# Kernel tuning notes

Hardware: AMD Instinct MI355X
Metric: run time of the kernel (lower is better)

## Reference

```python
import jax, jax.numpy as jnp
import numpy as np
import math

B, S, H, DM, DFF = 8, 512, 16, 1024, 4096
DK = DM // H
EPS = 1e-6


def setup_inputs() -> dict:
    key = jax.random.key(0)
    ks = jax.random.split(key, 12)
    rn = lambda k, shape, s=0.02: (jax.random.normal(k, shape, jnp.float32) * s)
    return dict(
        x=jax.random.normal(ks[0], (B, S, DM), jnp.float32),
        mask=jnp.ones((B, 1, 1, S), jnp.int32),
        Wq=rn(ks[1], (DM, DM)), bq=jnp.zeros((DM,), jnp.float32),
        Wk=rn(ks[2], (DM, DM)), bk=jnp.zeros((DM,), jnp.float32),
        Wv=rn(ks[3], (DM, DM)), bv=jnp.zeros((DM,), jnp.float32),
        Wo=rn(ks[4], (DM, DM)), bo=jnp.zeros((DM,), jnp.float32),
        r_k=rn(ks[5], (S, S, DK)),
        r_v=rn(ks[6], (S, S, DK)),
        ln1_g=jnp.ones((DM,), jnp.float32), ln1_b=jnp.zeros((DM,), jnp.float32),
        ln2_g=jnp.ones((DM,), jnp.float32), ln2_b=jnp.zeros((DM,), jnp.float32),
        w1=rn(ks[7], (DFF, DM)), b1=jnp.zeros((DFF,), jnp.float32),
        w2=rn(ks[8], (DM, DFF)), b2=jnp.zeros((DM,), jnp.float32),
    )


def _layernorm(x, g, b):
    # torch: std with Bessel correction (ddof=1), divide by (std + eps)
    mean = jnp.mean(x, axis=-1, keepdims=True)
    std = jnp.std(x, axis=-1, keepdims=True, ddof=1)
    return g * (x - mean) / (std + EPS) + b


def _gelu_tanh(x):
    c = math.sqrt(2.0 / math.pi)
    return 0.5 * x * (1.0 + jnp.tanh(c * (x + 0.044715 * x * x * x)))


def _attention(xn, mask, Wq, bq, Wk, bk, Wv, bv, Wo, bo, r_k, r_v):
    def heads(x, W, bias):
        y = x @ W.T + bias                      # [B,S,DM]
        return y.reshape(B, S, H, DK).transpose(0, 2, 1, 3)  # [B,H,S,DK]
    q, k, v = heads(xn, Wq, bq), heads(xn, Wk, bk), heads(xn, Wv, bv)
    scale = 1.0 / math.sqrt(DK)
    scores = jnp.einsum('bhqd,bhkd->bhqk', q, k) * scale
    rel_score = jnp.einsum('bhqd,qkd->bhqk', q, r_k)  # relative-position bias
    scores = scores + rel_score * scale
    scores = jnp.where(mask == 0, -1e9, scores)
    p = jax.nn.softmax(scores, axis=-1)
    out = jnp.einsum('bhqk,bhkd->bhqd', p, v) + jnp.einsum('bhqk,qkd->bhqd', p, r_v)
    out = out.transpose(0, 2, 1, 3).reshape(B, S, DM)
    return out @ Wo.T + bo


def reference(x, mask, Wq, bq, Wk, bk, Wv, bv, Wo, bo, r_k, r_v,
              ln1_g, ln1_b, ln2_g, ln2_b, w1, b1, w2, b2):
    # sublayer 1: x + attn(LN(x))
    x = x + _attention(_layernorm(x, ln1_g, ln1_b), mask,
                       Wq, bq, Wk, bk, Wv, bv, Wo, bo, r_k, r_v)
    # sublayer 2: x + FFN(LN(x))
    h = _layernorm(x, ln2_g, ln2_b)
    h = _gelu_tanh(h @ w1.T + b1) @ w2.T + b2
    return x + h
```

## Files before the change

### kernel.cpp

```cpp
#include <hip/hip_runtime.h>
#include <math.h>


typedef unsigned short ushort_t;
typedef __attribute__((ext_vector_type(8))) short short8;
typedef __attribute__((ext_vector_type(4))) float f32x4;
typedef __attribute__((ext_vector_type(8))) __bf16 bf16x8;

__device__ __forceinline__ float b2f(ushort_t u) {
  unsigned v = (unsigned)u << 16;
  return __builtin_bit_cast(float, v);
}
__device__ __forceinline__ ushort_t f2b(float f) {
  unsigned x = __builtin_bit_cast(unsigned, f);
  x = x + 0x7fffu + ((x >> 16) & 1u);
  return (ushort_t)(x >> 16);
}

__device__ __forceinline__ void gload16(const ushort_t* g, ushort_t* l) {
  __builtin_amdgcn_global_load_lds(
      (const __attribute__((address_space(1))) unsigned*)g,
      (__attribute__((address_space(3))) unsigned*)l, 16, 0, 0);
}

__global__ void k_f32_to_bf16(const float* __restrict__ in,
                              ushort_t* __restrict__ out, long long n) {
  long long i = ((long long)blockIdx.x * blockDim.x + threadIdx.x) * 4;
  if (i >= n) return;
  float4 v = *reinterpret_cast<const float4*>(in + i);
  ushort4 o;
  o.x = f2b(v.x); o.y = f2b(v.y); o.z = f2b(v.z); o.w = f2b(v.w);
  *reinterpret_cast<ushort4*>(out + i) = o;
}

__global__ void k_layernorm_bf16(const float* __restrict__ x,
                                 const float* __restrict__ g,
                                 const float* __restrict__ b,
                                 ushort_t* __restrict__ out) {
  const int lane = threadIdx.x & 63;
  const int row = (blockIdx.x << 2) + (threadIdx.x >> 6);
  const float* xr = x + (long long)row * 1024;
  float4 v[4];
  float s = 0.f, ss = 0.f;
#pragma unroll
  for (int i = 0; i < 4; ++i) {
    v[i] = *reinterpret_cast<const float4*>(xr + lane * 16 + i * 4);
    s += v[i].x + v[i].y + v[i].z + v[i].w;
    ss += v[i].x * v[i].x + v[i].y * v[i].y + v[i].z * v[i].z + v[i].w * v[i].w;
  }
#pragma unroll
  for (int o = 32; o > 0; o >>= 1) {
    s += __shfl_xor(s, o);
    ss += __shfl_xor(ss, o);
  }
  float mean = s * (1.f / 1024.f);
  float var = (ss - 1024.f * mean * mean) * (1.f / 1023.f);
  var = fmaxf(var, 0.f);
  float inv = 1.f / (sqrtf(var) + 1e-6f);
  ushort_t* orow = out + (long long)row * 1024;
#pragma unroll
  for (int i = 0; i < 4; ++i) {
    int c = lane * 16 + i * 4;
    ushort4 o;
    o.x = f2b(g[c + 0] * (v[i].x - mean) * inv + b[c + 0]);
    o.y = f2b(g[c + 1] * (v[i].y - mean) * inv + b[c + 1]);
    o.z = f2b(g[c + 2] * (v[i].z - mean) * inv + b[c + 2]);
    o.w = f2b(g[c + 3] * (v[i].w - mean) * inv + b[c + 3]);
    *reinterpret_cast<ushort4*>(orow + c) = o;
  }
}

__global__ void k_softmax(ushort_t* __restrict__ sc, const int* __restrict__ mask,
                          float scale) {
  const int lane = threadIdx.x & 63;
  const long long row = ((long long)blockIdx.x << 2) + (threadIdx.x >> 6);
  const int b = (int)(row >> 13);
  ushort_t* srow = sc + row * 512;
  const int* mrow = mask + b * 512;
  short8 sv = *reinterpret_cast<const short8*>(srow + lane * 8);
  float vals[8];
  float mx = -1e30f;
#pragma unroll
  for (int j = 0; j < 8; ++j) {
    float f = b2f((ushort_t)sv[j]) * scale;
    if (mrow[lane * 8 + j] == 0) f = -1e9f;
    vals[j] = f;
    mx = fmaxf(mx, f);
  }
#pragma unroll
  for (int o = 32; o > 0; o >>= 1) mx = fmaxf(mx, __shfl_xor(mx, o));
  float s = 0.f;
#pragma unroll
  for (int j = 0; j < 8; ++j) {
    vals[j] = __expf(vals[j] - mx);
    s += vals[j];
  }
#pragma unroll
  for (int o = 32; o > 0; o >>= 1) s += __shfl_xor(s, o);
  float inv = 1.f / s;
  short8 ov;
#pragma unroll
  for (int j = 0; j < 8; ++j) ov[j] = (short)f2b(vals[j] * inv);
  *reinterpret_cast<short8*>(srow + lane * 8) = ov;
}

__global__ void k_transpose_v(const ushort_t* __restrict__ v,
                              ushort_t* __restrict__ vT) {
  __shared__ ushort_t tls[64][72];
  const int bh = blockIdx.y;
  const int s0 = blockIdx.x << 6;
  const int t = threadIdx.x;
  const long long base = (long long)bh * 32768;
#pragma unroll
  for (int it = 0; it < 2; ++it) {
    int r = (t >> 3) + it * 32;
    int c = (t & 7) << 3;
    short8 val = *reinterpret_cast<const short8*>(v + base + (long long)(s0 + r) * 64 + c);
    *reinterpret_cast<short8*>(&tls[r][c]) = val;
  }
  __syncthreads();
#pragma unroll
  for (int it = 0; it < 2; ++it) {
    int d = (t >> 3) + it * 32;
    int cs = (t & 7) << 3;
    short8 o;
#pragma unroll
    for (int j = 0; j < 8; ++j) o[j] = (short)tls[cs + j][d];
    *reinterpret_cast<short8*>(vT + base + (long long)d * 512 + s0 + cs) = o;
  }
}

__global__ void k_transpose_rv(const float* __restrict__ rv,
                               ushort_t* __restrict__ rvT) {
  __shared__ float tls[64][65];
  const int q = blockIdx.y;
  const int k0 = blockIdx.x << 6;
  const int t = threadIdx.x;
  const long long ibase = (long long)q * 32768;
#pragma unroll
  for (int it = 0; it < 4; ++it) {
    int r = (t >> 4) + it * 16;
    int c = (t & 15) << 2;
    float4 val = *reinterpret_cast<const float4*>(rv + ibase + (long long)(k0 + r) * 64 + c);
    tls[r][c] = val.x; tls[r][c + 1] = val.y; tls[r][c + 2] = val.z; tls[r][c + 3] = val.w;
  }
  __syncthreads();
#pragma unroll
  for (int it = 0; it < 2; ++it) {
    int d = (t >> 3) + it * 32;
    int cs = (t & 7) << 3;
    short8 o;
#pragma unroll
    for (int j = 0; j < 8; ++j) o[j] = (short)f2b(tls[cs + j][d]);
    *reinterpret_cast<short8*>(rvT + ibase + (long long)d * 512 + k0 + cs) = o;
  }
}

__global__ void k_reshape_attn(const ushort_t* __restrict__ a,
                               ushort_t* __restrict__ o) {
  long long i = (long long)blockIdx.x * 256 + threadIdx.x;
  int col8 = (int)(i & 127);
  long long tok = i >> 7;
  int col = col8 << 3;
  int h = col >> 6, d = col & 63;
  int bb = (int)(tok >> 9), s = (int)(tok & 511);
  short8 v = *reinterpret_cast<const short8*>(
      a + ((long long)(bb * 16 + h) * 512 + s) * 64 + d);
  *reinterpret_cast<short8*>(o + (tok << 10) + col) = v;
}

struct GArgs {
  const ushort_t* A; const ushort_t* B;
  long long a_bs, b_bs, c_bs;
  long long a_rs, b_rs, c_rs;
  int M, N, K;
  float scale;
  ushort_t* Cb;
  float* Cf;
  const float* bias;
  const float* resid;
  ushort_t* qb; ushort_t* kb; ushort_t* vb;
  int swz;
};

template <int MODE>
__global__ __launch_bounds__(256) void k_gemm_bt(GArgs g) {
  __shared__ ushort_t As[2][128 * 32];
  __shared__ ushort_t Bs[2][128 * 32];
  const int t = threadIdx.x;
  const int lane = t & 63;
  const int w = t >> 6, wr = w >> 1, wc = w & 1;
  const long long z = blockIdx.z;

  int bx = blockIdx.x, by = blockIdx.y;
  if (g.swz) {
    int nx = gridDim.x;
    int id = by * nx + bx;
    int cpx = (nx * gridDim.y) >> 3;
    id = (id & 7) * cpx + (id >> 3);
    bx = id % nx;
    by = id / nx;
  }
  const int m0 = by * 128, n0 = bx * 128;

  const ushort_t* Ab = g.A + z * g.a_bs;
  const ushort_t* Bb = g.B + z * g.b_bs;
  const int sr = t >> 2;
  const int sc = (t & 3) << 3;
  const long long ar0 = min(m0 + sr, g.M - 1);
  const long long ar1 = min(m0 + sr + 64, g.M - 1);
  const long long br0 = min(n0 + sr, g.N - 1);
  const long long br1 = min(n0 + sr + 64, g.N - 1);
  const ushort_t* Ap0 = Ab + ar0 * g.a_rs + sc;
  const ushort_t* Ap1 = Ab + ar1 * g.a_rs + sc;
  const ushort_t* Bp0 = Bb + br0 * g.b_rs + sc;
  const ushort_t* Bp1 = Bb + br1 * g.b_rs + sc;
  const int wofs = w * 512;

  f32x4 acc[4][4];
#pragma unroll
  for (int i = 0; i < 4; ++i)
#pragma unroll
    for (int j = 0; j < 4; ++j) acc[i][j] = f32x4{0.f, 0.f, 0.f, 0.f};

  const int fr = lane & 15;
  const int fkb = (lane >> 4) << 3;
  const int a_off0 = (wr * 64 + fr) * 32 + fkb;
  const int b_off0 = (wc * 64 + fr) * 32 + fkb;

  const int nkt = g.K >> 5;
  gload16(Ap0, &As[0][wofs]);
  gload16(Ap1, &As[0][2048 + wofs]);
  gload16(Bp0, &Bs[0][wofs]);
  gload16(Bp1, &Bs[0][2048 + wofs]);

  for (int kt = 0; kt < nkt; ++kt) {
    const int cur = kt & 1;
    __syncthreads();
    if (kt + 1 < nkt) {
      const int k0 = (kt + 1) << 5;
      const int nxt = cur ^ 1;
      gload16(Ap0 + k0, &As[nxt][wofs]);
      gload16(Ap1 + k0, &As[nxt][2048 + wofs]);
      gload16(Bp0 + k0, &Bs[nxt][wofs]);
      gload16(Bp1 + k0, &Bs[nxt][2048 + wofs]);
    }
    bf16x8 af[4], bfv[4];
#pragma unroll
    for (int i = 0; i < 4; ++i)
      af[i] = *reinterpret_cast<const bf16x8*>(&As[cur][a_off0 + i * 512]);
#pragma unroll
    for (int j = 0; j < 4; ++j)
      bfv[j] = *reinterpret_cast<const bf16x8*>(&Bs[cur][b_off0 + j * 512]);
#pragma unroll
    for (int i = 0; i < 4; ++i)
#pragma unroll
      for (int j = 0; j < 4; ++j)
        acc[i][j] = __builtin_amdgcn_mfma_f32_16x16x32_bf16(af[i], bfv[j],
                                                            acc[i][j], 0, 0, 0);
  }

  const int er0 = wr * 64 + ((lane >> 4) << 2);
  const int ec0 = wc * 64 + (lane & 15);
#pragma unroll
  for (int i = 0; i < 4; ++i) {
#pragma unroll
    for (int j = 0; j < 4; ++j) {
#pragma unroll
      for (int r = 0; r < 4; ++r) {
        int row = m0 + er0 + i * 16 + r;
        int col = n0 + ec0 + j * 16;
        if (row >= g.M || col >= g.N) continue;
        float val = acc[i][j][r] * g.scale;
        if constexpr (MODE == 0) {
          g.Cb[z * g.c_bs + (long long)row * g.c_rs + col] = f2b(val);
        } else if constexpr (MODE == 1) {
          long long idx = z * g.c_bs + (long long)row * g.c_rs + col;
          g.Cb[idx] = f2b(b2f(g.Cb[idx]) + val);
        } else if constexpr (MODE == 2) {
          val += g.bias[col];
          int which = col >> 10;
          int h = (col >> 6) & 15;
          int d = col & 63;
          int bb = row >> 9, s = row & 511;
          ushort_t* dst = (which == 0) ? g.qb : (which == 1) ? g.kb : g.vb;
          dst[((long long)(bb * 16 + h) * 512 + s) * 64 + d] = f2b(val);
        } else if constexpr (MODE == 3) {
          long long idx = z * g.c_bs + (long long)row * g.c_rs + col;
          g.Cf[idx] = g.resid[idx] + val + g.bias[col];
        } else if constexpr (MODE == 4) {
          float xv = val + g.bias[col];
          float tv = tanhf(0.7978845608028654f * (xv + 0.044715f * xv * xv * xv));
          g.Cb[z * g.c_bs + (long long)row * g.c_rs + col] =
              f2b(0.5f * xv * (1.f + tv));
        }
      }
    }
  }
}

extern "C" void kernel_launch(void* const* d_in, const int* in_sizes, int n_in,
                              void* d_out, int out_size, void* d_ws,
                              size_t ws_size, hipStream_t stream) {
  const float* x    = (const float*)d_in[0];
  const int*   mask = (const int*)d_in[1];
  const float* Wq   = (const float*)d_in[2];
  const float* bq   = (const float*)d_in[3];
  const float* Wk   = (const float*)d_in[4];
  const float* bk   = (const float*)d_in[5];
  const float* Wv   = (const float*)d_in[6];
  const float* bv   = (const float*)d_in[7];
  const float* Wo   = (const float*)d_in[8];
  const float* bo   = (const float*)d_in[9];
  const float* r_k  = (const float*)d_in[10];
  const float* r_v  = (const float*)d_in[11];
  const float* ln1g = (const float*)d_in[12];
  const float* ln1b = (const float*)d_in[13];
  const float* ln2g = (const float*)d_in[14];
  const float* ln2b = (const float*)d_in[15];
  const float* w1   = (const float*)d_in[16];
  const float* b1   = (const float*)d_in[17];
  const float* w2   = (const float*)d_in[18];
  const float* b2   = (const float*)d_in[19];
  float* out = (float*)d_out;

  char* ws = (char*)d_ws;
  size_t off = 0;
  auto alloc = [&](size_t bytes) -> void* {
    void* p = ws + off;
    off += (bytes + 255) & ~(size_t)255;
    return p;
  };
  ushort_t* wqkv = (ushort_t*)alloc(3072ll * 1024 * 2);
  ushort_t* wo_b = (ushort_t*)alloc(1024ll * 1024 * 2);
  ushort_t* w1_b = (ushort_t*)alloc(4096ll * 1024 * 2);
  ushort_t* w2_b = (ushort_t*)alloc(1024ll * 4096 * 2);
  ushort_t* rk_b = (ushort_t*)alloc(512ll * 512 * 64 * 2);
  ushort_t* rvT  = (ushort_t*)alloc(512ll * 64 * 512 * 2);
  ushort_t* xn   = (ushort_t*)alloc(4096ll * 1024 * 2);
  ushort_t* qb   = (ushort_t*)alloc(128ll * 512 * 64 * 2);
  ushort_t* kb   = (ushort_t*)alloc(128ll * 512 * 64 * 2);
  ushort_t* vb   = (ushort_t*)alloc(128ll * 512 * 64 * 2);
  ushort_t* vT   = (ushort_t*)alloc(128ll * 64 * 512 * 2);
  ushort_t* scp  = (ushort_t*)alloc(128ll * 512 * 512 * 2);
  ushort_t* attn = (ushort_t*)alloc(128ll * 512 * 64 * 2);
  float*    x1   = (float*)alloc(4096ll * 1024 * 4);
  float*    bqkv = (float*)alloc(3072 * 4);
  ushort_t* attn_tok = xn;
  ushort_t* h_b = qb;
  ushort_t* mid = scp;

  hipMemcpyAsync(bqkv, bq, 1024 * 4, hipMemcpyDeviceToDevice, stream);
  hipMemcpyAsync(bqkv + 1024, bk, 1024 * 4, hipMemcpyDeviceToDevice, stream);
  hipMemcpyAsync(bqkv + 2048, bv, 1024 * 4, hipMemcpyDeviceToDevice, stream);

  auto cvt = [&](const float* src, ushort_t* dst, long long n) {
    k_f32_to_bf16<<<dim3((unsigned)((n / 4 + 255) / 256)), 256, 0, stream>>>(src, dst, n);
  };
  cvt(Wq, wqkv, 1024ll * 1024);
  cvt(Wk, wqkv + 1024ll * 1024, 1024ll * 1024);
  cvt(Wv, wqkv + 2048ll * 1024, 1024ll * 1024);
  cvt(Wo, wo_b, 1024ll * 1024);
  cvt(w1, w1_b, 4096ll * 1024);
  cvt(w2, w2_b, 1024ll * 4096);
  cvt(r_k, rk_b, 512ll * 512 * 64);
  k_transpose_rv<<<dim3(8, 512), 256, 0, stream>>>(r_v, rvT);

  k_layernorm_bf16<<<1024, 256, 0, stream>>>(x, ln1g, ln1b, xn);

  {
    GArgs a{};
    a.A = xn; a.B = wqkv; a.a_rs = 1024; a.b_rs = 1024;
    a.M = 4096; a.N = 3072; a.K = 1024; a.scale = 1.f;
    a.bias = bqkv; a.qb = qb; a.kb = kb; a.vb = vb; a.swz = 1;
    k_gemm_bt<2><<<dim3(24, 32, 1), 256, 0, stream>>>(a);
  }

  k_transpose_v<<<dim3(8, 128), 256, 0, stream>>>(vb, vT);

  {
    GArgs s{};
    s.A = qb; s.B = kb; s.a_bs = 32768; s.b_bs = 32768; s.c_bs = 262144;
    s.a_rs = 64; s.b_rs = 64; s.c_rs = 512;
    s.M = 512; s.N = 512; s.K = 64; s.scale = 1.f; s.Cb = scp;
    k_gemm_bt<0><<<dim3(4, 4, 128), 256, 0, stream>>>(s);
  }
  {
    GArgs r{};
    r.A = qb; r.B = rk_b; r.a_bs = 64; r.b_bs = 32768; r.c_bs = 512;
    r.a_rs = 32768; r.b_rs = 64; r.c_rs = 262144;
    r.M = 128; r.N = 512; r.K = 64; r.scale = 1.f; r.Cb = scp;
    k_gemm_bt<1><<<dim3(4, 1, 512), 256, 0, stream>>>(r);
  }

  k_softmax<<<16384, 256, 0, stream>>>(scp, mask, 0.125f);

  {
    GArgs pv{};
    pv.A = scp; pv.B = vT; pv.a_bs = 262144; pv.b_bs = 32768; pv.c_bs = 32768;
    pv.a_rs = 512; pv.b_rs = 512; pv.c_rs = 64;
    pv.M = 512; pv.N = 64; pv.K = 512; pv.scale = 1.f; pv.Cb = attn;
    k_gemm_bt<0><<<dim3(1, 4, 128), 256, 0, stream>>>(pv);
  }
  {
    GArgs pr{};
    pr.A = scp; pr.B = rvT; pr.a_bs = 512; pr.b_bs = 32768; pr.c_bs = 64;
    pr.a_rs = 262144; pr.b_rs = 512; pr.c_rs = 32768;
    pr.M = 128; pr.N = 64; pr.K = 512; pr.scale = 1.f; pr.Cb = attn;
    k_gemm_bt<1><<<dim3(1, 1, 512), 256, 0, stream>>>(pr);
  }

  k_reshape_attn<<<2048, 256, 0, stream>>>(attn, attn_tok);

  {
    GArgs o{};
    o.A = attn_tok; o.B = wo_b; o.a_rs = 1024; o.b_rs = 1024; o.c_rs = 1024;
    o.M = 4096; o.N = 1024; o.K = 1024; o.scale = 1.f;
    o.Cf = x1; o.bias = bo; o.resid = x; o.swz = 1;
    k_gemm_bt<3><<<dim3(8, 32, 1), 256, 0, stream>>>(o);
  }

  k_layernorm_bf16<<<1024, 256, 0, stream>>>(x1, ln2g, ln2b, h_b);

  {
    GArgs f1{};
    f1.A = h_b; f1.B = w1_b; f1.a_rs = 1024; f1.b_rs = 1024; f1.c_rs = 4096;
    f1.M = 4096; f1.N = 4096; f1.K = 1024; f1.scale = 1.f;
    f1.Cb = mid; f1.bias = b1; f1.swz = 1;
    k_gemm_bt<4><<<dim3(32, 32, 1), 256, 0, stream>>>(f1);
  }
  {
    GArgs f2{};
    f2.A = mid; f2.B = w2_b; f2.a_rs = 4096; f2.b_rs = 4096; f2.c_rs = 1024;
    f2.M = 4096; f2.N = 1024; f2.K = 4096; f2.scale = 1.f;
    f2.Cf = out; f2.bias = b2; f2.resid = x1; f2.swz = 1;
    k_gemm_bt<3><<<dim3(8, 32, 1), 256, 0, stream>>>(f2);
  }
}
```

Measured before the change: 600.5 us.

## Add 256x256-tile pipelined MFMA GEMM for the dense projection and FFN GEMMs

Adds a new GEMM kernel with 256x256 output tiles, 512 threads, 64-wide K steps and double-buffered LDS staging through global_load_lds. The LDS layout is XOR-swizzled and the loop interleaves loads with MFMA quarters using barriers and wait counts. It is used for the QKV, output projection and both FFN GEMMs to get more data reuse per tile and to hide memory latency. The cost is fewer blocks (64 for the N=1024 GEMMs), which risks underfilling the GPU's CUs. It also uses heavy register and LDS use with no bounds checks.

Result: slower. 618.0 us (+2.9%).

```diff
diff --git a/kernel.cpp b/kernel.cpp
--- a/kernel.cpp
+++ b/kernel.cpp
@@ -193,14 +193,6 @@
   const long long z = blockIdx.z;
 
   int bx = blockIdx.x, by = blockIdx.y;
-  if (g.swz) {
-    int nx = gridDim.x;
-    int id = by * nx + bx;
-    int cpx = (nx * gridDim.y) >> 3;
-    id = (id & 7) * cpx + (id >> 3);
-    bx = id % nx;
-    by = id / nx;
-  }
   const int m0 = by * 128, n0 = bx * 128;
 
   const ushort_t* Ab = g.A + z * g.a_bs;
@@ -277,7 +269,188 @@
         } else if constexpr (MODE == 1) {
           long long idx = z * g.c_bs + (long long)row * g.c_rs + col;
           g.Cb[idx] = f2b(b2f(g.Cb[idx]) + val);
-        } else if constexpr (MODE == 2) {
+        }
+      }
+    }
+  }
+}
+
+struct G2 {
+  const ushort_t* A; const ushort_t* B;
+  long long a_rs, b_rs, c_rs;
+  int K;
+  ushort_t* Cb; float* Cf;
+  const float* bias; const float* resid;
+  ushort_t* qb; ushort_t* kb; ushort_t* vb;
+};
+
+template <int MODE>
+__global__ __launch_bounds__(512, 2) void k_gemm256(G2 g) {
+  __shared__ ushort_t lds[65536];
+  const int t = threadIdx.x, lane = t & 63, w = t >> 6;
+  const int wm = w >> 2, wn = w & 3;
+
+  const int gx = gridDim.x;
+  int idx = blockIdx.y * gx + blockIdx.x;
+  const int cpx = (gx * gridDim.y) >> 3;
+  idx = (idx & 7) * cpx + (idx >> 3);
+  const int n0 = (idx % gx) * 256;
+  const int m0 = (idx / gx) * 256;
+
+  const int u0 = t, u1 = t + 512;
+  const ushort_t* Asrc0 = g.A + (long long)(m0 + (u0 >> 3)) * g.a_rs +
+                          (((u0 ^ ((u0 >> 3) & 7)) & 7) << 3);
+  const ushort_t* Asrc1 = g.A + (long long)(m0 + (u1 >> 3)) * g.a_rs +
+                          (((u1 ^ ((u1 >> 3) & 7)) & 7) << 3);
+  const ushort_t* Bsrc0 = g.B + (long long)(n0 + (u0 >> 3)) * g.b_rs +
+                          (((u0 ^ ((u0 >> 3) & 7)) & 7) << 3);
+  const ushort_t* Bsrc1 = g.B + (long long)(n0 + (u1 >> 3)) * g.b_rs +
+                          (((u1 ^ ((u1 >> 3) & 7)) & 7) << 3);
+
+  const int g4 = lane >> 4;
+  const int r15 = lane & 15;
+  const int sx = (lane & 7) << 4;
+  const int aoff0 = ((r15 * 128 + g4 * 16) ^ sx) >> 1;
+  const int aoff1 = ((r15 * 128 + 64 + g4 * 16) ^ sx) >> 1;
+  const int abase = wm * 8192;
+  const int bbase = 32768 + (wn >> 1) * 8192 + (wn & 1) * 4096;
+
+  f32x4 acc[8][4];
+#pragma unroll
+  for (int i = 0; i < 8; ++i)
+#pragma unroll
+    for (int j = 0; j < 4; ++j) acc[i][j] = f32x4{0.f, 0.f, 0.f, 0.f};
+  bf16x8 areg[8];
+  bf16x8 breg[8];
+
+  auto stageA = [&](int bsel, int h, int kt) {
+    long long ko = (long long)kt * 64 + (long long)h * 128 * g.a_rs;
+    gload16(Asrc0 + ko, &lds[bsel * 16384 + h * 8192 + w * 512]);
+    gload16(Asrc1 + ko, &lds[bsel * 16384 + h * 8192 + w * 512 + 4096]);
+  };
+  auto stageB = [&](int bsel, int h, int kt) {
+    long long ko = (long long)kt * 64 + (long long)h * 128 * g.b_rs;
+    gload16(Bsrc0 + ko, &lds[32768 + bsel * 16384 + h * 8192 + w * 512]);
+    gload16(Bsrc1 + ko, &lds[32768 + bsel * 16384 + h * 8192 + w * 512 + 4096]);
+  };
+  auto readA = [&](int bsel, int mh) {
+#pragma unroll
+    for (int f = 0; f < 4; ++f) {
+      const int base = bsel * 16384 + abase + (mh * 4 + f) * 1024;
+      areg[2 * f] = *reinterpret_cast<const bf16x8*>(&lds[base + aoff0]);
+      areg[2 * f + 1] = *reinterpret_cast<const bf16x8*>(&lds[base + aoff1]);
+    }
+  };
+  auto readB = [&](int bsel, int nh) {
+#pragma unroll
+    for (int nn = 0; nn < 2; ++nn) {
+      const int nf = nh * 2 + nn;
+      const int base = bsel * 16384 + bbase + nf * 1024;
+      breg[2 * nf] = *reinterpret_cast<const bf16x8*>(&lds[base + aoff0]);
+      breg[2 * nf + 1] = *reinterpret_cast<const bf16x8*>(&lds[base + aoff1]);
+    }
+  };
+  auto mmaQ = [&](int mh, int nh) {
+    __builtin_amdgcn_s_setprio(1);
+#pragma unroll
+    for (int f = 0; f < 4; ++f)
+#pragma unroll
+      for (int nn = 0; nn < 2; ++nn) {
+        const int an = mh * 4 + f, bn = nh * 2 + nn;
+#pragma unroll
+        for (int kk = 0; kk < 2; ++kk)
+          acc[an][bn] = __builtin_amdgcn_mfma_f32_16x16x32_bf16(
+              areg[2 * f + kk], breg[2 * bn + kk], acc[an][bn], 0, 0, 0);
+      }
+    __builtin_amdgcn_s_setprio(0);
+  };
+
+  const int nkt = g.K >> 6;
+  const int niter = nkt >> 1;
+
+  stageA(0, 0, 0); stageA(0, 1, 0);
+  stageB(0, 0, 0); stageB(0, 1, 0);
+  stageB(1, 0, 1); stageB(1, 1, 1);
+  asm volatile("s_waitcnt vmcnt(4)" ::: "memory");
+  __builtin_amdgcn_s_barrier();
+
+#pragma unroll 1
+  for (int it = 0; it < niter; ++it) {
+    const int kt0 = 2 * it;
+    const int ktb1 = kt0 + 1;
+    const int ktn0 = min(kt0 + 2, nkt - 1);
+    const int ktn1 = min(kt0 + 3, nkt - 1);
+
+    readA(0, 0); readB(0, 0);
+    stageA(1, 0, ktb1);
+    __builtin_amdgcn_s_barrier();
+    asm volatile("s_waitcnt lgkmcnt(0)" ::: "memory");
+    __builtin_amdgcn_sched_barrier(0);
+    mmaQ(0, 0);
+    __builtin_amdgcn_s_barrier();
+    readB(0, 1);
+    stageA(1, 1, ktb1);
+    __builtin_amdgcn_s_barrier();
+    asm volatile("s_waitcnt lgkmcnt(0)" ::: "memory");
+    __builtin_amdgcn_sched_barrier(0);
+    mmaQ(0, 1);
+    __builtin_amdgcn_s_barrier();
+    readA(0, 1);
+    stageB(0, 0, ktn0);
+    __builtin_amdgcn_s_barrier();
+    asm volatile("s_waitcnt lgkmcnt(0)" ::: "memory");
+    __builtin_amdgcn_sched_barrier(0);
+    mmaQ(1, 0);
+    __builtin_amdgcn_s_barrier();
+    stageB(0, 1, ktn0);
+    asm volatile("s_waitcnt vmcnt(4)" ::: "memory");
+    __builtin_amdgcn_s_barrier();
+    asm volatile("s_waitcnt lgkmcnt(0)" ::: "memory");
+    __builtin_amdgcn_sched_barrier(0);
+    mmaQ(1, 1);
+    __builtin_amdgcn_s_barrier();
+    readA(1, 0); readB(1, 0);
+    stageA(0, 0, ktn0);
+    __builtin_amdgcn_s_barrier();
+    asm volatile("s_waitcnt lgkmcnt(0)" ::: "memory");
+    __builtin_amdgcn_sched_barrier(0);
+    mmaQ(0, 0);
+    __builtin_amdgcn_s_barrier();
+    readB(1, 1);
+    stageA(0, 1, ktn0);
+    __builtin_amdgcn_s_barrier();
+    asm volatile("s_waitcnt lgkmcnt(0)" ::: "memory");
+    __builtin_amdgcn_sched_barrier(0);
+    mmaQ(0, 1);
+    __builtin_amdgcn_s_barrier();
+    readA(1, 1);
+    stageB(1, 0, ktn1);
+    __builtin_amdgcn_s_barrier();
+    asm volatile("s_waitcnt lgkmcnt(0)" ::: "memory");
+    __builtin_amdgcn_sched_barrier(0);
+    mmaQ(1, 0);
+    __builtin_amdgcn_s_barrier();
+    stageB(1, 1, ktn1);
+    asm volatile("s_waitcnt vmcnt(4)" ::: "memory");
+    __builtin_amdgcn_s_barrier();
+    asm volatile("s_waitcnt lgkmcnt(0)" ::: "memory");
+    __builtin_amdgcn_sched_barrier(0);
+    mmaQ(1, 1);
+    __builtin_amdgcn_s_barrier();
+  }
+
+  const int er = wm * 128 + ((lane >> 4) << 2);
+  const int ec = wn * 64 + (lane & 15);
+#pragma unroll
+  for (int f = 0; f < 8; ++f) {
+#pragma unroll
+    for (int nf = 0; nf < 4; ++nf) {
+#pragma unroll
+      for (int rr = 0; rr < 4; ++rr) {
+        const int row = m0 + er + f * 16 + rr;
+        const int col = n0 + ec + nf * 16;
+        float val = acc[f][nf][rr];
+        if constexpr (MODE == 2) {
           val += g.bias[col];
           int which = col >> 10;
           int h = (col >> 6) & 15;
@@ -286,13 +459,12 @@
           ushort_t* dst = (which == 0) ? g.qb : (which == 1) ? g.kb : g.vb;
           dst[((long long)(bb * 16 + h) * 512 + s) * 64 + d] = f2b(val);
         } else if constexpr (MODE == 3) {
-          long long idx = z * g.c_bs + (long long)row * g.c_rs + col;
+          long long idx = (long long)row * g.c_rs + col;
           g.Cf[idx] = g.resid[idx] + val + g.bias[col];
         } else if constexpr (MODE == 4) {
           float xv = val + g.bias[col];
           float tv = tanhf(0.7978845608028654f * (xv + 0.044715f * xv * xv * xv));
-          g.Cb[z * g.c_bs + (long long)row * g.c_rs + col] =
-              f2b(0.5f * xv * (1.f + tv));
+          g.Cb[(long long)row * g.c_rs + col] = f2b(0.5f * xv * (1.f + tv));
         }
       }
     }
@@ -369,11 +541,10 @@
   k_layernorm_bf16<<<1024, 256, 0, stream>>>(x, ln1g, ln1b, xn);
 
   {
-    GArgs a{};
-    a.A = xn; a.B = wqkv; a.a_rs = 1024; a.b_rs = 1024;
-    a.M = 4096; a.N = 3072; a.K = 1024; a.scale = 1.f;
-    a.bias = bqkv; a.qb = qb; a.kb = kb; a.vb = vb; a.swz = 1;
-    k_gemm_bt<2><<<dim3(24, 32, 1), 256, 0, stream>>>(a);
+    G2 a{};
+    a.A = xn; a.B = wqkv; a.a_rs = 1024; a.b_rs = 1024; a.K = 1024;
+    a.bias = bqkv; a.qb = qb; a.kb = kb; a.vb = vb;
+    k_gemm256<2><<<dim3(12, 16), 512, 0, stream>>>(a);
   }
 
   k_transpose_v<<<dim3(8, 128), 256, 0, stream>>>(vb, vT);
@@ -413,27 +584,24 @@
   k_reshape_attn<<<2048, 256, 0, stream>>>(attn, attn_tok);
 
   {
-    GArgs o{};
+    G2 o{};
     o.A = attn_tok; o.B = wo_b; o.a_rs = 1024; o.b_rs = 1024; o.c_rs = 1024;
-    o.M = 4096; o.N = 1024; o.K = 1024; o.scale = 1.f;
-    o.Cf = x1; o.bias = bo; o.resid = x; o.swz = 1;
-    k_gemm_bt<3><<<dim3(8, 32, 1), 256, 0, stream>>>(o);
+    o.K = 1024; o.Cf = x1; o.bias = bo; o.resid = x;
+    k_gemm256<3><<<dim3(4, 16), 512, 0, stream>>>(o);
   }
 
   k_layernorm_bf16<<<1024, 256, 0, stream>>>(x1, ln2g, ln2b, h_b);
 
   {
-    GArgs f1{};
+    G2 f1{};
     f1.A = h_b; f1.B = w1_b; f1.a_rs = 1024; f1.b_rs = 1024; f1.c_rs = 4096;
-    f1.M = 4096; f1.N = 4096; f1.K = 1024; f1.scale = 1.f;
-    f1.Cb = mid; f1.bias = b1; f1.swz = 1;
-    k_gemm_bt<4><<<dim3(32, 32, 1), 256, 0, stream>>>(f1);
-  }
-  {
-    GArgs f2{};
+    f1.K = 1024; f1.Cb = mid; f1.bias = b1;
+    k_gemm256<4><<<dim3(16, 16), 512, 0, stream>>>(f1);
+  }
+  {
+    G2 f2{};
     f2.A = mid; f2.B = w2_b; f2.a_rs = 4096; f2.b_rs = 4096; f2.c_rs = 1024;
-    f2.M = 4096; f2.N = 1024; f2.K = 4096; f2.scale = 1.f;
-    f2.Cf = out; f2.bias = b2; f2.resid = x1; f2.swz = 1;
-    k_gemm_bt<3><<<dim3(8, 32, 1), 256, 0, stream>>>(f2);
-  }
-}
+    f2.K = 4096; f2.Cf = out; f2.bias = b2; f2.resid = x1;
+    k_gemm256<3><<<dim3(4, 16), 512, 0, stream>>>(f2);
+  }
+}
```
